# Optimization experiments

Measured on AMD Instinct MI355X. Metric: run time of the kernel, lower is better.

The kernel has to match this reference:

```python
import jax, jax.numpy as jnp
import numpy as np

# hyp2f1 parameters of the Mann eddy-lifetime model: 2F1(1/3, 17/6, 4/3, -(kL)^-2)
A_P = 1.0 / 3.0
B_P = 17.0 / 6.0
C_P = 4.0 / 3.0
N_TERMS = 1000  # series terms; tail ~ N^{-2.5} -> ~1e-8 rel. error


def _hyp2f1_pfaff_series(w):
    """2F1(1/3, -3/2, 4/3, w) for w in [0, 1] via its power series.

    This is the Pfaff-transformed series; terms decay like n^{-3.5} * w^n,
    so a fixed N_TERMS truncation is accurate over the whole range.
    """
    a, bp, c = A_P, C_P - B_P, C_P  # bp = -3/2

    def body(carry, n):
        s, term = carry
        term = term * ((a + n) * (bp + n)) / ((c + n) * (n + 1.0)) * w
        return (s + term, term), None

    init = (jnp.ones_like(w), jnp.ones_like(w))
    (s, _), _ = jax.lax.scan(body, init, jnp.arange(N_TERMS, dtype=w.dtype))
    return s


def _mann_hyp2f1(t):
    """2F1(1/3, 17/6, 4/3, -t^-2) for t > 0 via the Pfaff transformation.

    2F1(a,b,c,z) = (1-z)^{-a} 2F1(a, c-b, c, z/(z-1)) with z = -1/t^2,
    so z/(z-1) = 1/(1+t^2) in (0,1) and (1-z) = (1+t^2)/t^2.
    """
    t2 = t * t
    w = 1.0 / (1.0 + t2)
    pref = (t2 * w) ** A_P  # (1-z)^{-a}
    return pref * _hyp2f1_pfaff_series(w)


def setup_inputs() -> dict:
    key = jax.random.key(0)
    k = jax.random.normal(key, (256, 256, 128, 3), dtype=jnp.float32)
    L = jnp.ones((), dtype=jnp.float32)
    gamma = jnp.ones((), dtype=jnp.float32)
    return {"k": k, "L": L, "gamma": gamma}


def reference(k, L, gamma):
    # Original detaches k and L (tau is non-differentiable); only gamma carries grad.
    k_s = jax.lax.stop_gradient(k)
    L_s = jax.lax.stop_gradient(L)
    k_norm = jnp.linalg.norm(k_s, axis=-1)  # [256,256,128]
    kL = L_s * k_norm
    mask = kL > 0.0
    safe_t = jnp.where(mask, kL, 1.0)
    F = _mann_hyp2f1(safe_t)
    tau = jnp.where(mask, safe_t ** (-2.0 / 3.0) / jnp.sqrt(F), 0.0)
    return gamma * tau
```

## Files before the change

### kernel.cpp

```cpp
#include <hip/hip_runtime.h>
#include <math.h>


typedef float f4 __attribute__((ext_vector_type(4)));

constexpr int NT = 48;

struct CoefArr { float v[NT]; };

constexpr CoefArr gen_coefs() {
    CoefArr r{};
    double term = 1.0;
    r.v[0] = 1.0f;
    for (int n = 0; n + 1 < NT; ++n) {
        const double a  = 1.0 / 3.0;
        const double bp = -1.5;
        const double c  = 4.0 / 3.0;
        term *= ((a + n) * (bp + n)) / ((c + n) * (n + 1.0));
        r.v[n + 1] = (float)term;
    }
    return r;
}

constexpr CoefArr COEF = gen_coefs();

__device__ __forceinline__ float mann_tau(float t2) {
    float w = __builtin_amdgcn_rcpf(1.0f + t2);
    float s = COEF.v[NT - 1];
#pragma unroll
    for (int n = NT - 2; n >= 0; --n) s = fmaf(s, w, COEF.v[n]);
    float cw = __builtin_amdgcn_exp2f(__builtin_amdgcn_logf(w) * (1.0f / 3.0f));
    return __builtin_amdgcn_rsqf(t2 * cw * s);
}

__global__ __launch_bounds__(256) void mann_elt_kernel(
    const float* __restrict__ k,
    const float* __restrict__ Lp,
    const float* __restrict__ gp,
    float* __restrict__ out,
    int n)
{
    const int  gid  = blockIdx.x * blockDim.x + threadIdx.x;
    const long base = (long)gid * 8;
    if (base >= n) return;

    const float L  = Lp[0];
    const float g  = gp[0];
    const float L2 = L * L;

    if (base + 7 < (long)n) {
        const f4* k4 = (const f4*)k + (size_t)gid * 6;
        float f[24];
#pragma unroll
        for (int j = 0; j < 6; ++j) {
            f4 v = __builtin_nontemporal_load(&k4[j]);
            f[4 * j + 0] = v[0];
            f[4 * j + 1] = v[1];
            f[4 * j + 2] = v[2];
            f[4 * j + 3] = v[3];
        }

        float res[8];
#pragma unroll
        for (int j = 0; j < 8; ++j) {
            float x = f[3 * j + 0];
            float y = f[3 * j + 1];
            float z = f[3 * j + 2];
            float t2  = L2 * fmaf(x, x, fmaf(y, y, z * z));
            float tau = mann_tau(t2);
            res[j] = (t2 > 0.0f) ? g * tau : 0.0f;
        }

        f4 o0 = (f4){res[0], res[1], res[2], res[3]};
        f4 o1 = (f4){res[4], res[5], res[6], res[7]};
        f4* o4 = (f4*)(out + base);
        __builtin_nontemporal_store(o0, o4 + 0);
        __builtin_nontemporal_store(o1, o4 + 1);
    } else {
        for (int j = 0; j < 8 && base + j < (long)n; ++j) {
            const long i = base + j;
            float kx = k[3 * i + 0];
            float ky = k[3 * i + 1];
            float kz = k[3 * i + 2];
            float t2  = L2 * (kx * kx + ky * ky + kz * kz);
            float tau = mann_tau(t2);
            out[i] = (t2 > 0.0f) ? g * tau : 0.0f;
        }
    }
}

extern "C" void kernel_launch(void* const* d_in, const int* in_sizes, int n_in,
                              void* d_out, int out_size, void* d_ws, size_t ws_size,
                              hipStream_t stream) {
    const float* k  = (const float*)d_in[0];
    const float* L  = (const float*)d_in[1];
    const float* g  = (const float*)d_in[2];
    float* out = (float*)d_out;

    const int n  = out_size;
    const int n8 = (n + 7) / 8;
    const int block = 256;
    const int grid  = (n8 + block - 1) / block;

    mann_elt_kernel<<<grid, block, 0, stream>>>(k, L, g, out, n);
}
```

Baseline: 172.6 us.

## Stage input through LDS for coalesced loads, process four points per thread

Result: faster. 155.2 us (-10.1%).

```diff
diff --git a/kernel.cpp b/kernel.cpp
--- a/kernel.cpp
+++ b/kernel.cpp
@@ -40,45 +40,47 @@
     float* __restrict__ out,
     int n)
 {
-    const int  gid  = blockIdx.x * blockDim.x + threadIdx.x;
-    const long base = (long)gid * 8;
-    if (base >= n) return;
+    const int  t        = threadIdx.x;
+    const long blockPts = (long)blockIdx.x * 1024;
 
     const float L  = Lp[0];
     const float g  = gp[0];
     const float L2 = L * L;
 
-    if (base + 7 < (long)n) {
-        const f4* k4 = (const f4*)k + (size_t)gid * 6;
-        float f[24];
+    __shared__ f4 sk4[768];
+
+    if (blockPts + 1024 <= (long)n) {
+        const f4* kg    = (const f4*)k;
+        const long base4 = blockPts * 3 / 4;
 #pragma unroll
-        for (int j = 0; j < 6; ++j) {
-            f4 v = __builtin_nontemporal_load(&k4[j]);
-            f[4 * j + 0] = v[0];
-            f[4 * j + 1] = v[1];
-            f[4 * j + 2] = v[2];
-            f[4 * j + 3] = v[3];
+        for (int i = 0; i < 3; ++i)
+            sk4[t + i * 256] = kg[base4 + t + i * 256];
+        __syncthreads();
+
+        const float* skf = (const float*)sk4;
+        const f4*    sp  = (const f4*)(skf + t * 12);
+        f4 p0 = sp[0];
+        f4 p1 = sp[1];
+        f4 p2 = sp[2];
+
+        float n2[4];
+        n2[0] = fmaf(p0[0], p0[0], fmaf(p0[1], p0[1], p0[2] * p0[2]));
+        n2[1] = fmaf(p0[3], p0[3], fmaf(p1[0], p1[0], p1[1] * p1[1]));
+        n2[2] = fmaf(p1[2], p1[2], fmaf(p1[3], p1[3], p2[0] * p2[0]));
+        n2[3] = fmaf(p2[1], p2[1], fmaf(p2[2], p2[2], p2[3] * p2[3]));
+
+        f4 o;
+#pragma unroll
+        for (int j = 0; j < 4; ++j) {
+            float t2  = L2 * n2[j];
+            float tau = mann_tau(t2);
+            o[j] = (t2 > 0.0f) ? g * tau : 0.0f;
         }
-
-        float res[8];
-#pragma unroll
-        for (int j = 0; j < 8; ++j) {
-            float x = f[3 * j + 0];
-            float y = f[3 * j + 1];
-            float z = f[3 * j + 2];
-            float t2  = L2 * fmaf(x, x, fmaf(y, y, z * z));
-            float tau = mann_tau(t2);
-            res[j] = (t2 > 0.0f) ? g * tau : 0.0f;
-        }
-
-        f4 o0 = (f4){res[0], res[1], res[2], res[3]};
-        f4 o1 = (f4){res[4], res[5], res[6], res[7]};
-        f4* o4 = (f4*)(out + base);
-        __builtin_nontemporal_store(o0, o4 + 0);
-        __builtin_nontemporal_store(o1, o4 + 1);
+        __builtin_nontemporal_store(o, (f4*)(out + blockPts) + t);
     } else {
-        for (int j = 0; j < 8 && base + j < (long)n; ++j) {
-            const long i = base + j;
+        for (int j = 0; j < 4; ++j) {
+            const long i = blockPts + (long)t * 4 + j;
+            if (i >= (long)n) break;
             float kx = k[3 * i + 0];
             float ky = k[3 * i + 1];
             float kz = k[3 * i + 2];
@@ -97,10 +99,10 @@
     const float* g  = (const float*)d_in[2];
     float* out = (float*)d_out;
 
-    const int n  = out_size;
-    const int n8 = (n + 7) / 8;
+    const int n = out_size;
     const int block = 256;
-    const int grid  = (n8 + block - 1) / block;
+    const int ptsPerBlock = 1024;
+    const int grid = (n + ptsPerBlock - 1) / ptsPerBlock;
 
     mann_elt_kernel<<<grid, block, 0, stream>>>(k, L, g, out, n);
 }
```
